# Kernel optimization log

Measured on AMD Instinct MI355X. Metric: run time of the kernel, lower is better.

The kernel has to match this reference:

```python
import jax, jax.numpy as jnp
import numpy as np
from jax import lax

V = 50000          # vocab
E = 64             # embedding_dim
B = 64             # batch
SEQ = 1024         # sentence length
NC = 6             # num_classes
L = 4              # num_layers (total conv layers)
KTOP = 4
NF = [10, 14, 18, 22]          # num_filters per stage
KS = [7, 5, 5, 3]              # kernel sizes
ROWS = [E // 2**i for i in range(5)]   # [64,32,16,8,4]
GROUPS = ROWS[:4]              # conv_i groups = rows[i-1]
# dynamic k-max schedule: k_l = max(k_top, ceil((L-l)/L * SEQ)) for l=1,2,3; last pool uses k_top
KPOOL = [max(KTOP, int(np.ceil((L - l) / L * SEQ))) for l in (1, 2, 3)] + [KTOP]  # [768,512,256,4]


def _uniform(key, shape, fan):
    s = 1.0 / np.sqrt(fan)
    return jax.random.uniform(key, shape, jnp.float32, -s, s)


def setup_inputs() -> dict:
    key = jax.random.key(0)
    ks = jax.random.split(key, 16)
    tokens = jax.random.randint(ks[0], (B, SEQ), 0, V)
    emb = jax.random.normal(ks[1], (V, E), jnp.float32)
    inp = {"tokens": tokens, "emb": emb}
    # conv weights: OIH layout, I = in_channels / groups = num_filters[i-1] (or 1 for conv1)
    in_pg = [1, NF[0], NF[1], NF[2]]
    out_ch = [NF[i] * ROWS[i] for i in range(4)]   # [640,448,288,176]
    for i in range(4):
        fan = in_pg[i] * KS[i]
        inp[f"w{i+1}"] = _uniform(ks[2 + 2 * i], (out_ch[i], in_pg[i], KS[i]), fan)
        inp[f"b{i+1}"] = _uniform(ks[3 + 2 * i], (out_ch[i],), fan)
    fc_in = ROWS[4] * NF[3] * KTOP   # 4*22*4 = 352
    inp["fcw"] = _uniform(ks[10], (NC, fc_in), fc_in)
    inp["fcb"] = _uniform(ks[11], (NC,), fc_in)
    return inp


def _fold(x, nf):
    # channel index c = row*nf + filt; sum adjacent rows pairwise (Fold(2,2))
    b, d, s = x.shape
    r = d // nf
    return x.reshape(b, r // 2, 2, nf, s).sum(axis=2).reshape(b, d // 2, s)


def _kmax(x, k):
    # top-k along seq axis, preserving original temporal order
    _, idx = lax.top_k(x, k)
    idx = jnp.sort(idx, axis=-1)
    return jnp.take_along_axis(x, idx, axis=-1)


def reference(tokens, emb, w1, b1, w2, b2, w3, b3, w4, b4, fcw, fcb):
    x = emb[tokens]                 # (B, S, E)
    x = x.transpose(0, 2, 1)        # (B, E, S)
    ws, bs = (w1, w2, w3, w4), (b1, b2, b3, b4)
    for i in range(4):
        pad = KS[i] - 1             # 'wide' convolution
        x = lax.conv_general_dilated(
            x, ws[i], (1,), [(pad, pad)],
            dimension_numbers=("NCH", "OIH", "NCH"),
            feature_group_count=GROUPS[i],
        ) + bs[i][None, :, None]
        x = _fold(x, NF[i])
        x = _kmax(x, KPOOL[i])
        x = jnp.tanh(x)
    # dropout is identity in eval mode
    x = x.reshape(x.shape[0], -1)   # (B, 352)
    return x @ fcw.T + fcb
```

## Files before the change

kernel.cpp:

```cpp
#include <hip/hip_runtime.h>
#include <hip/hip_bf16.h>
#include <math.h>


#if defined(__has_builtin)
#if __has_builtin(__builtin_amdgcn_ballot_w64)
#define BALLOT64(expr) __builtin_amdgcn_ballot_w64(expr)
#endif
#endif
#ifndef BALLOT64
#define BALLOT64(expr) __ballot(expr)
#endif

__device__ __forceinline__ unsigned f2ord(float f) {
    unsigned u = __float_as_uint(f);
    return (u & 0x80000000u) ? ~u : (u | 0x80000000u);
}
__device__ __forceinline__ float ord2f(unsigned key) {
    unsigned u = (key & 0x80000000u) ? (key & 0x7fffffffu) : ~key;
    return __uint_as_float(u);
}
__device__ __forceinline__ float tanh_fast(float x) {
    float e = __expf(2.f * x);
    return 1.f - 2.f * __builtin_amdgcn_rcpf(e + 1.f);
}
__device__ __forceinline__ int mbcnt64(unsigned long long m) {
    return __builtin_amdgcn_mbcnt_hi((unsigned)(m >> 32),
           __builtin_amdgcn_mbcnt_lo((unsigned)m, 0u));
}

template<int CH>
__device__ __forceinline__ void select_finish(const unsigned* keys, unsigned T,
                                              int k, float* __restrict__ out)
{
    int g = 0, e = 0;
    #pragma unroll
    for (int i = 0; i < CH; ++i) { g += (keys[i] > T); e += (keys[i] == T); }

    int gtBefore = 0, eqBefore = 0, totG = 0;
    #pragma unroll
    for (int b = 0; b < 5; ++b) {
        unsigned long long mg = BALLOT64((((g >> b) & 1) != 0));
        unsigned long long me = BALLOT64((((e >> b) & 1) != 0));
        gtBefore += mbcnt64(mg) << b;
        eqBefore += mbcnt64(me) << b;
        totG     += __popcll(mg) << b;
    }
    const int needTies = k - totG;

    int gRun = 0, eRun = 0;
    #pragma unroll
    for (int i = 0; i < CH; ++i) {
        const unsigned key = keys[i];
        const bool isG = key > T;
        const bool isE = key == T;
        const int eIdx = eqBefore + eRun;
        const int dst = gtBefore + gRun + min(eIdx, needTies);
        if (isG || (isE && eIdx < needTies))
            out[dst] = tanh_fast(ord2f(key));
        gRun += isG; eRun += isE;
    }
}

template<int N, int CH>
__device__ void wave_selectN(const unsigned (*keys)[CH], int k,
                             float* const* outs)
{
    unsigned p[N];
    int above[N], buck[N];
    #pragma unroll
    for (int n = 0; n < N; ++n) { p[n] = 0u; above[n] = 0; buck[n] = 64 * CH; }

    unsigned doneMask = 0;
    const unsigned allDone = (1u << N) - 1u;
    #pragma unroll 1
    for (int pos = 31; pos >= 0; --pos) {
        #pragma unroll
        for (int n = 0; n < N; ++n) {
            if (!((doneMask >> n) & 1u)) {
                const unsigned t = p[n] | (1u << pos);
                int c = 0;
                #pragma unroll
                for (int i = 0; i < CH; ++i)
                    c += __popcll(BALLOT64((keys[n][i] >= t)));
                const int inb = c - above[n];
                const int rem = k - above[n];
                if (inb >= rem) { p[n] = t; buck[n] = inb; }
                else            { above[n] += inb; buck[n] -= inb; }
                if (buck[n] == k - above[n]) doneMask |= (1u << n);
            }
        }
        if (doneMask == allDone) break;
    }
    #pragma unroll
    for (int n = 0; n < N; ++n)
        select_finish<CH>(keys[n], p[n], k, outs[n]);
}

__global__ __launch_bounds__(128) void layer1_fused(
    const int* __restrict__ tokens, const float* __restrict__ emb,
    const float* __restrict__ W1, const float* __restrict__ B1,
    float* __restrict__ Z1)
{
    const int j = blockIdx.x;
    const int b = blockIdx.y;
    const int t = threadIdx.x;
    const int w = t >> 6;
    const int lane = t & 63;

    __shared__ float xr[2][1100];

    const float2* emb2 = (const float2*)emb;
    for (int i = t; i < 1100; i += 128) {
        int s = i - 6;
        float a = 0.f, c = 0.f;
        if (s >= 0 && s < 1024) {
            int tok = tokens[b * 1024 + s];
            float2 v = emb2[(size_t)tok * 32 + j];
            a = v.x; c = v.y;
        }
        xr[0][i] = a;
        xr[1][i] = c;
    }
    __syncthreads();

    const int beg = lane * 17;

    unsigned keys[5][17];
    float* outs[5];
    const size_t orow = (size_t)b * 320 + (size_t)j * 10;

    #pragma unroll
    for (int q = 0; q < 5; ++q) {
        const int f = 5 * w + q;
        float wa[7], wb[7];
        #pragma unroll
        for (int k2 = 0; k2 < 7; ++k2) {
            wa[k2] = W1[(2 * j * 10 + f) * 7 + k2];
            wb[k2] = W1[((2 * j + 1) * 10 + f) * 7 + k2];
        }
        const float bias = B1[2 * j * 10 + f] + B1[(2 * j + 1) * 10 + f];
        #pragma unroll
        for (int i = 0; i < 17; ++i) {
            float acc = bias;
            #pragma unroll
            for (int k2 = 0; k2 < 7; ++k2)
                acc += xr[0][beg + i + k2] * wa[k2]
                     + xr[1][beg + i + k2] * wb[k2];
            keys[q][i] = (beg + i < 1030) ? f2ord(acc) : 0u;
        }
        outs[q] = Z1 + (orow + f) * 768;
    }
    wave_selectN<5, 17>(keys, 768, outs);
}

template <int IPG, int NF, int K, int SIN, int SOUT, int KSEL, int NW, int CH>
__global__ __launch_bounds__(NW * 64) void conv_fold_select_kernel(
    const float* __restrict__ X, const float* __restrict__ W,
    const float* __restrict__ Bias, float* __restrict__ Z,
    int Cin, int Cfold)
{
    static_assert(NF == 2 * NW, "2 filters per wave");
    static_assert(64 * CH >= SOUT, "chunk covers row");
    constexpr int W2 = 64 * CH + K - 1;

    const int t = threadIdx.x;
    const int j = blockIdx.x;
    const int b = blockIdx.y;
    const int wav = t >> 6, lane = t & 63;

    __shared__ float xs[2 * IPG][W2];

    const float* Xb = X + ((size_t)b * Cin + (size_t)(2 * j) * IPG) * SIN;
    for (int idx = t; idx < 2 * IPG * W2; idx += NW * 64) {
        int r = idx / W2, p = idx - r * W2;
        int sg = p - (K - 1);
        xs[r][p] = (sg >= 0 && sg < SIN) ? Xb[(size_t)r * SIN + sg] : 0.f;
    }
    __syncthreads();

    const int f0 = __builtin_amdgcn_readfirstlane(2 * wav);
    float acc0[CH], acc1[CH];
    {
        float bias0 = Bias[2 * j * NF + f0]     + Bias[(2 * j + 1) * NF + f0];
        float bias1 = Bias[2 * j * NF + f0 + 1] + Bias[(2 * j + 1) * NF + f0 + 1];
        #pragma unroll
        for (int i = 0; i < CH; ++i) { acc0[i] = bias0; acc1[i] = bias1; }
    }
    const int base = lane * CH;

    #pragma unroll 2
    for (int h = 0; h < 2; ++h) {
        const float* Wh = W + (size_t)((2 * j + h) * NF) * IPG * K;
        #pragma unroll 1
        for (int c = 0; c < IPG; ++c) {
            float win[CH + K - 1];
            #pragma unroll
            for (int p = 0; p < CH + K - 1; ++p)
                win[p] = xs[h * IPG + c][base + p];
            #pragma unroll
            for (int k2 = 0; k2 < K; ++k2) {
                const float w0 = Wh[((size_t)f0 * IPG + c) * K + k2];
                const float w1 = Wh[((size_t)(f0 + 1) * IPG + c) * K + k2];
                #pragma unroll
                for (int i = 0; i < CH; ++i) {
                    acc0[i] = fmaf(win[i + k2], w0, acc0[i]);
                    acc1[i] = fmaf(win[i + k2], w1, acc1[i]);
                }
            }
        }
    }

    unsigned keys[2][CH];
    #pragma unroll
    for (int i = 0; i < CH; ++i) {
        keys[0][i] = (base + i < SOUT) ? f2ord(acc0[i]) : 0u;
        keys[1][i] = (base + i < SOUT) ? f2ord(acc1[i]) : 0u;
    }
    const size_t orow = (size_t)b * Cfold + (size_t)j * NF;
    float* outs[2] = { Z + (orow + f0) * (size_t)KSEL,
                       Z + (orow + f0 + 1) * (size_t)KSEL };
    wave_selectN<2, CH>(keys, KSEL, outs);
}

__global__ __launch_bounds__(192) void fc_kernel(
    const float* __restrict__ Z, const float* __restrict__ Wf,
    const float* __restrict__ bf, float* __restrict__ out)
{
    int g = blockIdx.x * blockDim.x + threadIdx.x;
    if (g >= 64 * 6) return;
    int b = g / 6, c = g % 6;
    float acc = bf[c];
    const float* zr = Z + b * 352;
    const float* wr = Wf + c * 352;
    for (int i = 0; i < 352; ++i) acc += zr[i] * wr[i];
    out[g] = acc;
}

extern "C" void kernel_launch(void* const* d_in, const int* in_sizes, int n_in,
                              void* d_out, int out_size, void* d_ws, size_t ws_size,
                              hipStream_t stream)
{
    const int*   tokens = (const int*)  d_in[0];
    const float* emb    = (const float*)d_in[1];
    const float* w1     = (const float*)d_in[2];
    const float* b1     = (const float*)d_in[3];
    const float* w2     = (const float*)d_in[4];
    const float* b2     = (const float*)d_in[5];
    const float* w3     = (const float*)d_in[6];
    const float* b3     = (const float*)d_in[7];
    const float* w4     = (const float*)d_in[8];
    const float* b4     = (const float*)d_in[9];
    const float* fcw    = (const float*)d_in[10];
    const float* fcb    = (const float*)d_in[11];
    float* out = (float*)d_out;
    float* ws  = (float*)d_ws;

    float* Z1 = ws;
    float* Z2 = ws + 15728640;
    float* Z3 = ws;
    float* Z4 = ws + 2359296;

    layer1_fused<<<dim3(32, 64), 128, 0, stream>>>(tokens, emb, w1, b1, Z1);

    conv_fold_select_kernel<10, 14, 5, 768, 772, 512, 7, 13>
        <<<dim3(16, 64), 7 * 64, 0, stream>>>(Z1, w2, b2, Z2, 320, 224);

    conv_fold_select_kernel<14, 18, 5, 512, 516, 256, 9, 9>
        <<<dim3(8, 64), 9 * 64, 0, stream>>>(Z2, w3, b3, Z3, 224, 144);

    conv_fold_select_kernel<18, 22, 3, 256, 258, 4, 11, 5>
        <<<dim3(4, 64), 11 * 64, 0, stream>>>(Z3, w4, b4, Z4, 144, 88);

    fc_kernel<<<2, 192, 0, stream>>>(Z4, fcw, fcb, out);
}
```

Measured before the change: 370.5 us.

## Stage k-max outputs in LDS for coalesced stores and phase layer-2 input loads

Selected top-k values are now written scattered into a per-wave shared-memory buffer and then copied out to global memory in lane-contiguous order, replacing scattered global stores with coalesced ones. The conv kernel also gains a PHASES parameter that loads input rows into LDS in several passes, halving shared memory for layer 2 so more blocks fit per CU. The cost is extra LDS traffic, an added barrier per phase, and extra staging buffers that raise LDS use in the other kernels. The staging copy relies on wave-level ordering and has no explicit barrier between the scattered writes and the read-back.

```diff
diff --git a/kernel.cpp b/kernel.cpp
--- a/kernel.cpp
+++ b/kernel.cpp
@@ -31,7 +31,8 @@
 
 template<int CH>
 __device__ __forceinline__ void select_finish(const unsigned* keys, unsigned T,
-                                              int k, float* __restrict__ out)
+                                              int k, float* stage,
+                                              float* __restrict__ out)
 {
     int g = 0, e = 0;
     #pragma unroll
@@ -57,13 +58,16 @@
         const int eIdx = eqBefore + eRun;
         const int dst = gtBefore + gRun + min(eIdx, needTies);
         if (isG || (isE && eIdx < needTies))
-            out[dst] = tanh_fast(ord2f(key));
+            stage[dst] = tanh_fast(ord2f(key));
         gRun += isG; eRun += isE;
     }
+    const int lane = threadIdx.x & 63;
+    for (int i = lane; i < k; i += 64)
+        out[i] = stage[i];
 }
 
 template<int N, int CH>
-__device__ void wave_selectN(const unsigned (*keys)[CH], int k,
+__device__ void wave_selectN(const unsigned (*keys)[CH], int k, float* stage,
                              float* const* outs)
 {
     unsigned p[N];
@@ -94,7 +98,7 @@
     }
     #pragma unroll
     for (int n = 0; n < N; ++n)
-        select_finish<CH>(keys[n], p[n], k, outs[n]);
+        select_finish<CH>(keys[n], p[n], k, stage, outs[n]);
 }
 
 __global__ __launch_bounds__(128) void layer1_fused(
@@ -109,6 +113,7 @@
     const int lane = t & 63;
 
     __shared__ float xr[2][1100];
+    __shared__ float stagebuf[2][768];
 
     const float2* emb2 = (const float2*)emb;
     for (int i = t; i < 1100; i += 128) {
@@ -151,10 +156,11 @@
         }
         outs[q] = Z1 + (orow + f) * 768;
     }
-    wave_selectN<5, 17>(keys, 768, outs);
-}
-
-template <int IPG, int NF, int K, int SIN, int SOUT, int KSEL, int NW, int CH>
+    wave_selectN<5, 17>(keys, 768, stagebuf[w], outs);
+}
+
+template <int IPG, int NF, int K, int SIN, int SOUT, int KSEL, int NW, int CH,
+          int PHASES>
 __global__ __launch_bounds__(NW * 64) void conv_fold_select_kernel(
     const float* __restrict__ X, const float* __restrict__ W,
     const float* __restrict__ Bias, float* __restrict__ Z,
@@ -163,21 +169,17 @@
     static_assert(NF == 2 * NW, "2 filters per wave");
     static_assert(64 * CH >= SOUT, "chunk covers row");
     constexpr int W2 = 64 * CH + K - 1;
+    constexpr int RS = 2 * IPG / PHASES;
 
     const int t = threadIdx.x;
     const int j = blockIdx.x;
     const int b = blockIdx.y;
     const int wav = t >> 6, lane = t & 63;
 
-    __shared__ float xs[2 * IPG][W2];
+    __shared__ float xs[RS][W2];
+    __shared__ float stagebuf[NW][KSEL];
 
     const float* Xb = X + ((size_t)b * Cin + (size_t)(2 * j) * IPG) * SIN;
-    for (int idx = t; idx < 2 * IPG * W2; idx += NW * 64) {
-        int r = idx / W2, p = idx - r * W2;
-        int sg = p - (K - 1);
-        xs[r][p] = (sg >= 0 && sg < SIN) ? Xb[(size_t)r * SIN + sg] : 0.f;
-    }
-    __syncthreads();
 
     const int f0 = __builtin_amdgcn_readfirstlane(2 * wav);
     float acc0[CH], acc1[CH];
@@ -189,25 +191,36 @@
     }
     const int base = lane * CH;
 
-    #pragma unroll 2
-    for (int h = 0; h < 2; ++h) {
-        const float* Wh = W + (size_t)((2 * j + h) * NF) * IPG * K;
+    #pragma unroll 1
+    for (int ph = 0; ph < PHASES; ++ph) {
+        if (ph) __syncthreads();
+        for (int idx = t; idx < RS * W2; idx += NW * 64) {
+            int r = idx / W2, p = idx - r * W2;
+            int sg = p - (K - 1);
+            int gr = ph * RS + r;
+            xs[r][p] = (sg >= 0 && sg < SIN) ? Xb[(size_t)gr * SIN + sg] : 0.f;
+        }
+        __syncthreads();
+
+        int h = (ph * RS) / IPG, c = (ph * RS) % IPG;
         #pragma unroll 1
-        for (int c = 0; c < IPG; ++c) {
+        for (int r = 0; r < RS; ++r) {
             float win[CH + K - 1];
             #pragma unroll
             for (int p = 0; p < CH + K - 1; ++p)
-                win[p] = xs[h * IPG + c][base + p];
+                win[p] = xs[r][base + p];
+            const float* Wp = W + ((size_t)((2 * j + h) * NF + f0) * IPG + c) * K;
             #pragma unroll
             for (int k2 = 0; k2 < K; ++k2) {
-                const float w0 = Wh[((size_t)f0 * IPG + c) * K + k2];
-                const float w1 = Wh[((size_t)(f0 + 1) * IPG + c) * K + k2];
+                const float w0 = Wp[k2];
+                const float w1 = Wp[(size_t)IPG * K + k2];
                 #pragma unroll
                 for (int i = 0; i < CH; ++i) {
                     acc0[i] = fmaf(win[i + k2], w0, acc0[i]);
                     acc1[i] = fmaf(win[i + k2], w1, acc1[i]);
                 }
             }
+            if (++c == IPG) { c = 0; ++h; }
         }
     }
 
@@ -220,7 +233,7 @@
     const size_t orow = (size_t)b * Cfold + (size_t)j * NF;
     float* outs[2] = { Z + (orow + f0) * (size_t)KSEL,
                        Z + (orow + f0 + 1) * (size_t)KSEL };
-    wave_selectN<2, CH>(keys, KSEL, outs);
+    wave_selectN<2, CH>(keys, KSEL, stagebuf[wav], outs);
 }
 
 __global__ __launch_bounds__(192) void fc_kernel(
@@ -263,13 +276,13 @@
 
     layer1_fused<<<dim3(32, 64), 128, 0, stream>>>(tokens, emb, w1, b1, Z1);
 
-    conv_fold_select_kernel<10, 14, 5, 768, 772, 512, 7, 13>
+    conv_fold_select_kernel<10, 14, 5, 768, 772, 512, 7, 13, 2>
         <<<dim3(16, 64), 7 * 64, 0, stream>>>(Z1, w2, b2, Z2, 320, 224);
 
-    conv_fold_select_kernel<14, 18, 5, 512, 516, 256, 9, 9>
+    conv_fold_select_kernel<14, 18, 5, 512, 516, 256, 9, 9, 1>
         <<<dim3(8, 64), 9 * 64, 0, stream>>>(Z2, w3, b3, Z3, 224, 144);
 
-    conv_fold_select_kernel<18, 22, 3, 256, 258, 4, 11, 5>
+    conv_fold_select_kernel<18, 22, 3, 256, 258, 4, 11, 5, 1>
         <<<dim3(4, 64), 11 * 64, 0, stream>>>(Z3, w4, b4, Z4, 144, 88);
 
     fc_kernel<<<2, 192, 0, stream>>>(Z4, fcw, fcb, out);
```

New measurement: 343.1 us. 7.4% less time.
